# Kernel optimization log

Measured on AMD Instinct MI355X. Metric: run time of the kernel, lower is better.

Reference implementation:

```python
import jax, jax.numpy as jnp
import numpy as np
import math

D_MODEL = 32
N_HEADS = 2
FEAT_DIM = 16
HEAD_DIM = 16  # d_model // num_key_value_heads
EPS = 1e-12
R2 = math.sqrt(2.0)
RD = math.sqrt(FEAT_DIM)
RRD = math.sqrt(RD)


def taylor_exp(x):
    # x: (b, h, l, f) -> (b, h, l, 1 + f + f*f)
    b, h, l, f = x.shape
    x2 = (x[..., :, None] * x[..., None, :]).reshape(b, h, l, f * f) / R2
    term1 = jnp.ones_like(x[..., :1])
    term2 = x / RRD
    term3 = x2 / RD
    return jnp.concatenate([term1, term2, term3], axis=-1)


def setup_inputs() -> dict:
    key = jax.random.key(0)
    ks = jax.random.split(key, 5)
    b, l = 4, 2048
    return {
        "hidden_states": jax.random.normal(ks[0], (b, l, D_MODEL), dtype=jnp.float32),
        "Wq": jax.random.normal(ks[1], (FEAT_DIM * N_HEADS, D_MODEL), dtype=jnp.float32) * (1.0 / math.sqrt(D_MODEL)),
        "Wk": jax.random.normal(ks[2], (FEAT_DIM * N_HEADS, D_MODEL), dtype=jnp.float32) * (1.0 / math.sqrt(D_MODEL)),
        "Wv": jax.random.normal(ks[3], (N_HEADS * HEAD_DIM, D_MODEL), dtype=jnp.float32) * (1.0 / math.sqrt(D_MODEL)),
        "Wo": jax.random.normal(ks[4], (D_MODEL, N_HEADS * HEAD_DIM), dtype=jnp.float32) * (1.0 / math.sqrt(D_MODEL)),
    }


def reference(hidden_states, Wq, Wk, Wv, Wo):
    b, l, _ = hidden_states.shape
    # projections (nn.Linear: x @ W.T)
    q = (hidden_states @ Wq.T).reshape(b, l, N_HEADS, FEAT_DIM).transpose(0, 2, 1, 3)  # (b,h,l,f)
    k = (hidden_states @ Wk.T).reshape(b, l, N_HEADS, FEAT_DIM).transpose(0, 2, 1, 3)
    v = (hidden_states @ Wv.T).reshape(b, l, N_HEADS, HEAD_DIM).transpose(0, 2, 1, 3)  # (b,h,l,d)

    q = taylor_exp(q)  # (b,h,l,D) with D = 1+f+f^2 = 273
    k = taylor_exp(k)

    # causal linear attention: num_t = q_t . sum_{s<=t} k_s v_s^T
    kv = jnp.cumsum(k[..., None, :] * v[..., :, None], axis=2)  # (b,h,l,d,D)
    num = jnp.einsum('bhlD,bhldD->bhld', q, kv)                  # (b,h,l,d)
    denom = jnp.einsum('bhlD,bhlD->bhl', q, jnp.cumsum(k, axis=2)) + EPS
    y = num / denom[..., None]

    y = y.transpose(0, 2, 1, 3).reshape(b, l, N_HEADS * HEAD_DIM)  # (b,l,h*d)
    return (y @ Wo.T).astype(hidden_states.dtype)
```

## Files before the change

kernel.cpp:

```cpp
#include <hip/hip_runtime.h>
#include <math.h>

#define B 4
#define H 2
#define L 2048
#define DM 32
#define F 16
#define HD 16
#define DD 273
#define CHK 64
#define NC (L / CHK)
#define BH (B * H)

#define SC_LIN 0.5f
#define SC_QUAD 0.17677669529663687f

__global__ __launch_bounds__(256) void chunksum_kernel(
    const float* __restrict__ hs, const float* __restrict__ Wq,
    const float* __restrict__ Wk, const float* __restrict__ Wv,
    float* __restrict__ qp, float* __restrict__ kp, float* __restrict__ vp,
    float* __restrict__ S_kv, float* __restrict__ S_k) {
  int blk = blockIdx.x;
  int bh = blk >> 5, ch = blk & (NC - 1);
  int b = bh >> 1, h = bh & 1;
  int lane = threadIdx.x & 63, wave = threadIdx.x >> 6;
  int l = ch * CHK + lane;

  __shared__ float ks[CHK][F + 1];
  __shared__ float vs[CHK][F];

  float x[DM];
  const float4* xr = (const float4*)(hs + ((size_t)b * L + l) * DM);
#pragma unroll
  for (int j = 0; j < DM / 4; j++) {
    float4 v = xr[j];
    x[4 * j] = v.x; x[4 * j + 1] = v.y; x[4 * j + 2] = v.z; x[4 * j + 3] = v.w;
  }
  for (int c = wave * 12; c < wave * 12 + 12; c++) {
    int kind = c >> 4;
    int f = c & 15;
    const float* __restrict__ W = (kind == 0) ? Wq : (kind == 1) ? Wk : Wv;
    const float* wr = W + (size_t)(h * 16 + f) * DM;
    float acc = 0.f;
#pragma unroll
    for (int i = 0; i < DM; i++) acc += x[i] * wr[i];
    float* dst = (kind == 0) ? qp : (kind == 1) ? kp : vp;
    dst[((size_t)bh * L + l) * F + f] = acc;
    if (kind == 1) ks[lane][f] = acc;
    if (kind == 2) vs[lane][f] = acc;
  }
  if (threadIdx.x < CHK) ks[threadIdx.x][16] = 1.0f;
  __syncthreads();

#pragma unroll
  for (int rep = 0; rep < 2; rep++) {
    int dd = threadIdx.x + rep * 256;
    if (dd >= DD) break;
    int i, j;
    float sc;
    if (dd == 0) {
      i = 16; j = 16; sc = 1.0f;
    } else if (dd <= F) {
      i = dd - 1; j = 16; sc = SC_LIN;
    } else {
      int m = dd - 17;
      i = m >> 4; j = m & 15; sc = SC_QUAD;
    }
    float acc[HD];
#pragma unroll
    for (int hh = 0; hh < HD; hh++) acc[hh] = 0.f;
    float acck = 0.f;
    for (int p = 0; p < CHK; p++) {
      float kf = sc * ks[p][i] * ks[p][j];
      acck += kf;
      const float4* vr = (const float4*)vs[p];
#pragma unroll
      for (int h4 = 0; h4 < 4; h4++) {
        float4 v = vr[h4];
        acc[4 * h4] += kf * v.x;
        acc[4 * h4 + 1] += kf * v.y;
        acc[4 * h4 + 2] += kf * v.z;
        acc[4 * h4 + 3] += kf * v.w;
      }
    }
    float* dst = S_kv + ((size_t)blk * DD + dd) * HD;
#pragma unroll
    for (int hh = 0; hh < HD; hh++) dst[hh] = acc[hh];
    S_k[(size_t)blk * DD + dd] = acck;
  }
}

#define PSLICES 19
__global__ __launch_bounds__(256) void prefix_kernel(float* __restrict__ S_kv,
                                                     float* __restrict__ S_k) {
  int blk = blockIdx.x;
  int bh = blk / PSLICES, sl = blk % PSLICES;
  int e = sl * 256 + threadIdx.x;
  if (e < DD * HD) {
    size_t base = (size_t)bh * NC * DD * HD + e;
    float v[NC];
#pragma unroll
    for (int c = 0; c < NC; c++) v[c] = S_kv[base + (size_t)c * DD * HD];
    float run = 0.f;
#pragma unroll
    for (int c = 0; c < NC; c++) {
      S_kv[base + (size_t)c * DD * HD] = run;
      run += v[c];
    }
  } else if (e < DD * HD + DD) {
    int e2 = e - DD * HD;
    size_t base = (size_t)bh * NC * DD + e2;
    float v[NC];
#pragma unroll
    for (int c = 0; c < NC; c++) v[c] = S_k[base + (size_t)c * DD];
    float run = 0.f;
#pragma unroll
    for (int c = 0; c < NC; c++) {
      S_k[base + (size_t)c * DD] = run;
      run += v[c];
    }
  }
}

__global__ __launch_bounds__(256) void outchunk_kernel(
    const float* __restrict__ qp, const float* __restrict__ kp,
    const float* __restrict__ vp, const float* __restrict__ St_kv,
    const float* __restrict__ St_k, float* __restrict__ y) {
  int blk = blockIdx.x;
  int bh = blk >> 5, ch = blk & (NC - 1);
  int b = bh >> 1, h = bh & 1;
  int t = threadIdx.x & 63;
  int u = threadIdx.x >> 6;

  __shared__ float qs[CHK][F + 1];
  __shared__ float ks[CHK][F];
  __shared__ float vs[CHK][F];
  __shared__ float S[DD][HD];
  __shared__ float Sk[DD + 3];
  __shared__ float red[4][CHK][20];

  const float4* qb = (const float4*)(qp + ((size_t)bh * L + (size_t)ch * CHK) * F);
  const float4* kb = (const float4*)(kp + ((size_t)bh * L + (size_t)ch * CHK) * F);
  const float4* vb = (const float4*)(vp + ((size_t)bh * L + (size_t)ch * CHK) * F);
  {
    int r = threadIdx.x >> 2, c4 = (threadIdx.x & 3) * 4;
    float4 v = qb[threadIdx.x];
    qs[r][c4] = v.x; qs[r][c4 + 1] = v.y; qs[r][c4 + 2] = v.z; qs[r][c4 + 3] = v.w;
    ((float4*)ks)[threadIdx.x] = kb[threadIdx.x];
    ((float4*)vs)[threadIdx.x] = vb[threadIdx.x];
  }
  if (threadIdx.x < CHK) qs[threadIdx.x][16] = 1.0f;
  const float4* Sb = (const float4*)(St_kv + (size_t)blk * DD * HD);
  for (int i = threadIdx.x; i < DD * HD / 4; i += 256) ((float4*)S)[i] = Sb[i];
  const float* Skb = St_k + (size_t)blk * DD;
  for (int i = threadIdx.x; i < DD; i += 256) Sk[i] = Skb[i];

  float qreg[F];
  const float4* qrow = (const float4*)(qp + ((size_t)bh * L + (size_t)ch * CHK + t) * F);
#pragma unroll
  for (int j = 0; j < 4; j++) {
    float4 v = qrow[j];
    qreg[4 * j] = v.x; qreg[4 * j + 1] = v.y;
    qreg[4 * j + 2] = v.z; qreg[4 * j + 3] = v.w;
  }
  __syncthreads();

  float acc[HD];
#pragma unroll
  for (int hh = 0; hh < HD; hh++) acc[hh] = 0.f;
  float den = 0.f;

  for (int dd = u; dd < DD; dd += 4) {
    float phi;
    if (dd == 0) {
      phi = 1.0f;
    } else if (dd <= F) {
      phi = qs[t][dd - 1] * SC_LIN;
    } else {
      int m = dd - 17;
      phi = qs[t][m >> 4] * qs[t][m & 15] * SC_QUAD;
    }
    den += phi * Sk[dd];
    const float4* Sr = (const float4*)S[dd];
#pragma unroll
    for (int j4 = 0; j4 < 4; j4++) {
      float4 sv = Sr[j4];
      acc[4 * j4] += phi * sv.x;
      acc[4 * j4 + 1] += phi * sv.y;
      acc[4 * j4 + 2] += phi * sv.z;
      acc[4 * j4 + 3] += phi * sv.w;
    }
  }

#pragma unroll
  for (int m = 0; m < CHK / 4; m++) {
    int s = u + 4 * m;
    const float4* kr = (const float4*)ks[s];
    float dot = 0.f;
#pragma unroll
    for (int i4 = 0; i4 < 4; i4++) {
      float4 kv = kr[i4];
      dot += qreg[4 * i4] * kv.x + qreg[4 * i4 + 1] * kv.y +
             qreg[4 * i4 + 2] * kv.z + qreg[4 * i4 + 3] * kv.w;
    }
    float scv = 1.0f + dot * 0.25f + dot * dot * 0.03125f;
    scv = (s <= t) ? scv : 0.0f;
    den += scv;
    const float4* vr = (const float4*)vs[s];
#pragma unroll
    for (int h4 = 0; h4 < 4; h4++) {
      float4 v = vr[h4];
      acc[4 * h4] += scv * v.x;
      acc[4 * h4 + 1] += scv * v.y;
      acc[4 * h4 + 2] += scv * v.z;
      acc[4 * h4 + 3] += scv * v.w;
    }
  }

#pragma unroll
  for (int hh = 0; hh < HD; hh++) red[u][t][hh] = acc[hh];
  red[u][t][16] = den;
  __syncthreads();

  for (int idx = threadIdx.x; idx < CHK * 17; idx += 256) {
    int t2 = idx / 17, e = idx % 17;
    red[0][t2][e] =
        red[0][t2][e] + red[1][t2][e] + red[2][t2][e] + red[3][t2][e];
  }
  __syncthreads();

  if (threadIdx.x < CHK) {
    int t2 = threadIdx.x;
    float inv = 1.0f / (red[0][t2][16] + 1e-12f);
    float* yb = y + (((size_t)(b * L + ch * CHK + t2)) * H + h) * HD;
#pragma unroll
    for (int hh = 0; hh < HD; hh++) yb[hh] = red[0][t2][hh] * inv;
  }
}

__global__ __launch_bounds__(256) void out_kernel(const float* __restrict__ y,
                                                  const float* __restrict__ Wo,
                                                  float* __restrict__ out) {
  int lane = threadIdx.x & 63;
  int wave = threadIdx.x >> 6;
  int row = blockIdx.x * 64 + lane;
  float yr[DM];
  const float4* yb = (const float4*)(y + (size_t)row * DM);
#pragma unroll
  for (int j = 0; j < DM / 4; j++) {
    float4 v = yb[j];
    yr[4 * j] = v.x; yr[4 * j + 1] = v.y; yr[4 * j + 2] = v.z; yr[4 * j + 3] = v.w;
  }
  for (int c = wave * 8; c < wave * 8 + 8; c++) {
    float acc = 0.f;
#pragma unroll
    for (int i = 0; i < DM; i++) acc += yr[i] * Wo[c * DM + i];
    out[(size_t)row * DM + c] = acc;
  }
}

extern "C" void kernel_launch(void* const* d_in, const int* in_sizes, int n_in,
                              void* d_out, int out_size, void* d_ws,
                              size_t ws_size, hipStream_t stream) {
  const float* hs = (const float*)d_in[0];
  const float* Wq = (const float*)d_in[1];
  const float* Wk = (const float*)d_in[2];
  const float* Wv = (const float*)d_in[3];
  const float* Wo = (const float*)d_in[4];
  float* out = (float*)d_out;

  float* ws = (float*)d_ws;
  float* qp = ws;
  float* kp = qp + (size_t)BH * L * F;
  float* vp = kp + (size_t)BH * L * F;
  float* S_kv = vp + (size_t)BH * L * F;
  float* S_k = S_kv + (size_t)BH * NC * DD * HD;
  float* y = S_k + (size_t)BH * NC * DD;

  chunksum_kernel<<<BH * NC, 256, 0, stream>>>(hs, Wq, Wk, Wv, qp, kp, vp,
                                               S_kv, S_k);
  prefix_kernel<<<BH * PSLICES, 256, 0, stream>>>(S_kv, S_k);
  outchunk_kernel<<<BH * NC, 256, 0, stream>>>(qp, kp, vp, S_kv, S_k, y);
  out_kernel<<<B * L / 64, 256, 0, stream>>>(y, Wo, out);
}
```

Measured before the change: 106.9 us.

## Split projection into own kernel and read S/k/v via uniform global loads

Moves the QKV projection out of chunksum into a separate proj_kernel that computes both heads per row, removing duplicate hidden-state reads. chunksum and outchunk now read v, k, S and Sk directly from global memory through wave-uniform addresses (readfirstlane) instead of staging them in LDS, so the loads can become scalar loads. outchunk grows to 512 threads with 8 waves splitting the DD and intra-chunk loops, which cuts LDS use and adds parallelism. The cost is an extra kernel launch and dependence on scalar-cache behaviour.

New measurement: 106.5 us. Within noise of the previous version (-0.4%).

```diff
diff --git a/kernel.cpp b/kernel.cpp
--- a/kernel.cpp
+++ b/kernel.cpp
@@ -15,42 +15,56 @@
 #define SC_LIN 0.5f
 #define SC_QUAD 0.17677669529663687f
 
-__global__ __launch_bounds__(256) void chunksum_kernel(
+__global__ __launch_bounds__(256) void proj_kernel(
     const float* __restrict__ hs, const float* __restrict__ Wq,
     const float* __restrict__ Wk, const float* __restrict__ Wv,
-    float* __restrict__ qp, float* __restrict__ kp, float* __restrict__ vp,
+    float* __restrict__ qp, float* __restrict__ kp, float* __restrict__ vp) {
+  int lane = threadIdx.x & 63;
+  int wave = __builtin_amdgcn_readfirstlane(threadIdx.x >> 6);
+  int rg = blockIdx.x >> 1;
+  int half = blockIdx.x & 1;
+  int row = rg * 64 + lane;
+  int b = row >> 11, l = row & (L - 1);
+
+  float x[DM];
+  const float4* xr = (const float4*)(hs + (size_t)row * DM);
+#pragma unroll
+  for (int j = 0; j < DM / 4; j++) {
+    float4 v = xr[j];
+    x[4 * j] = v.x; x[4 * j + 1] = v.y; x[4 * j + 2] = v.z; x[4 * j + 3] = v.w;
+  }
+  int c0 = half * 48 + wave * 12;
+  for (int c = c0; c < c0 + 12; c++) {
+    int kind = c >> 5;
+    int cc = c & 31;
+    const float* __restrict__ W = (kind == 0) ? Wq : (kind == 1) ? Wk : Wv;
+    const float* __restrict__ wr = W + (size_t)cc * DM;
+    float acc = 0.f;
+#pragma unroll
+    for (int i = 0; i < DM; i++) acc += x[i] * wr[i];
+    int h = cc >> 4, f = cc & 15;
+    float* dst = (kind == 0) ? qp : (kind == 1) ? kp : vp;
+    dst[(((size_t)(b * H + h) * L) + l) * F + f] = acc;
+  }
+}
+
+__global__ __launch_bounds__(256) void chunksum_kernel(
+    const float* __restrict__ kp, const float* __restrict__ vp,
     float* __restrict__ S_kv, float* __restrict__ S_k) {
   int blk = blockIdx.x;
   int bh = blk >> 5, ch = blk & (NC - 1);
-  int b = bh >> 1, h = bh & 1;
-  int lane = threadIdx.x & 63, wave = threadIdx.x >> 6;
-  int l = ch * CHK + lane;
-
   __shared__ float ks[CHK][F + 1];
-  __shared__ float vs[CHK][F];
-
-  float x[DM];
-  const float4* xr = (const float4*)(hs + ((size_t)b * L + l) * DM);
-#pragma unroll
-  for (int j = 0; j < DM / 4; j++) {
-    float4 v = xr[j];
-    x[4 * j] = v.x; x[4 * j + 1] = v.y; x[4 * j + 2] = v.z; x[4 * j + 3] = v.w;
-  }
-  for (int c = wave * 12; c < wave * 12 + 12; c++) {
-    int kind = c >> 4;
-    int f = c & 15;
-    const float* __restrict__ W = (kind == 0) ? Wq : (kind == 1) ? Wk : Wv;
-    const float* wr = W + (size_t)(h * 16 + f) * DM;
-    float acc = 0.f;
-#pragma unroll
-    for (int i = 0; i < DM; i++) acc += x[i] * wr[i];
-    float* dst = (kind == 0) ? qp : (kind == 1) ? kp : vp;
-    dst[((size_t)bh * L + l) * F + f] = acc;
-    if (kind == 1) ks[lane][f] = acc;
-    if (kind == 2) vs[lane][f] = acc;
+
+  const float4* kb = (const float4*)(kp + ((size_t)bh * L + (size_t)ch * CHK) * F);
+  {
+    int r = threadIdx.x >> 2, c4 = (threadIdx.x & 3) * 4;
+    float4 v = kb[threadIdx.x];
+    ks[r][c4] = v.x; ks[r][c4 + 1] = v.y; ks[r][c4 + 2] = v.z; ks[r][c4 + 3] = v.w;
   }
   if (threadIdx.x < CHK) ks[threadIdx.x][16] = 1.0f;
   __syncthreads();
+
+  const float* __restrict__ vbase = vp + ((size_t)bh * L + (size_t)ch * CHK) * F;
 
 #pragma unroll
   for (int rep = 0; rep < 2; rep++) {
@@ -73,15 +87,9 @@
     for (int p = 0; p < CHK; p++) {
       float kf = sc * ks[p][i] * ks[p][j];
       acck += kf;
-      const float4* vr = (const float4*)vs[p];
-#pragma unroll
-      for (int h4 = 0; h4 < 4; h4++) {
-        float4 v = vr[h4];
-        acc[4 * h4] += kf * v.x;
-        acc[4 * h4 + 1] += kf * v.y;
-        acc[4 * h4 + 2] += kf * v.z;
-        acc[4 * h4 + 3] += kf * v.w;
-      }
+      const float* __restrict__ vr = vbase + p * F;
+#pragma unroll
+      for (int hh = 0; hh < HD; hh++) acc[hh] += kf * vr[hh];
     }
     float* dst = S_kv + ((size_t)blk * DD + dd) * HD;
 #pragma unroll
@@ -122,7 +130,7 @@
   }
 }
 
-__global__ __launch_bounds__(256) void outchunk_kernel(
+__global__ __launch_bounds__(512) void outchunk_kernel(
     const float* __restrict__ qp, const float* __restrict__ kp,
     const float* __restrict__ vp, const float* __restrict__ St_kv,
     const float* __restrict__ St_k, float* __restrict__ y) {
@@ -130,33 +138,23 @@
   int bh = blk >> 5, ch = blk & (NC - 1);
   int b = bh >> 1, h = bh & 1;
   int t = threadIdx.x & 63;
-  int u = threadIdx.x >> 6;
+  int u = __builtin_amdgcn_readfirstlane(threadIdx.x >> 6);
 
   __shared__ float qs[CHK][F + 1];
-  __shared__ float ks[CHK][F];
-  __shared__ float vs[CHK][F];
-  __shared__ float S[DD][HD];
-  __shared__ float Sk[DD + 3];
-  __shared__ float red[4][CHK][20];
-
-  const float4* qb = (const float4*)(qp + ((size_t)bh * L + (size_t)ch * CHK) * F);
-  const float4* kb = (const float4*)(kp + ((size_t)bh * L + (size_t)ch * CHK) * F);
-  const float4* vb = (const float4*)(vp + ((size_t)bh * L + (size_t)ch * CHK) * F);
-  {
+  __shared__ float red[8][CHK][21];
+
+  if (threadIdx.x < 256) {
+    const float4* qb =
+        (const float4*)(qp + ((size_t)bh * L + (size_t)ch * CHK) * F);
     int r = threadIdx.x >> 2, c4 = (threadIdx.x & 3) * 4;
     float4 v = qb[threadIdx.x];
     qs[r][c4] = v.x; qs[r][c4 + 1] = v.y; qs[r][c4 + 2] = v.z; qs[r][c4 + 3] = v.w;
-    ((float4*)ks)[threadIdx.x] = kb[threadIdx.x];
-    ((float4*)vs)[threadIdx.x] = vb[threadIdx.x];
-  }
-  if (threadIdx.x < CHK) qs[threadIdx.x][16] = 1.0f;
-  const float4* Sb = (const float4*)(St_kv + (size_t)blk * DD * HD);
-  for (int i = threadIdx.x; i < DD * HD / 4; i += 256) ((float4*)S)[i] = Sb[i];
-  const float* Skb = St_k + (size_t)blk * DD;
-  for (int i = threadIdx.x; i < DD; i += 256) Sk[i] = Skb[i];
+    if (threadIdx.x < CHK) qs[threadIdx.x][16] = 1.0f;
+  }
 
   float qreg[F];
-  const float4* qrow = (const float4*)(qp + ((size_t)bh * L + (size_t)ch * CHK + t) * F);
+  const float4* qrow =
+      (const float4*)(qp + ((size_t)bh * L + (size_t)ch * CHK + t) * F);
 #pragma unroll
   for (int j = 0; j < 4; j++) {
     float4 v = qrow[j];
@@ -170,51 +168,42 @@
   for (int hh = 0; hh < HD; hh++) acc[hh] = 0.f;
   float den = 0.f;
 
-  for (int dd = u; dd < DD; dd += 4) {
+  const float* __restrict__ Sbase = St_kv + (size_t)blk * DD * HD;
+  const float* __restrict__ Skb = St_k + (size_t)blk * DD;
+
+  for (int m = 0; m < 35; m++) {
+    int dd = u + (m << 3);
+    if (dd >= DD) break;
     float phi;
     if (dd == 0) {
       phi = 1.0f;
     } else if (dd <= F) {
       phi = qs[t][dd - 1] * SC_LIN;
     } else {
-      int m = dd - 17;
-      phi = qs[t][m >> 4] * qs[t][m & 15] * SC_QUAD;
-    }
-    den += phi * Sk[dd];
-    const float4* Sr = (const float4*)S[dd];
-#pragma unroll
-    for (int j4 = 0; j4 < 4; j4++) {
-      float4 sv = Sr[j4];
-      acc[4 * j4] += phi * sv.x;
-      acc[4 * j4 + 1] += phi * sv.y;
-      acc[4 * j4 + 2] += phi * sv.z;
-      acc[4 * j4 + 3] += phi * sv.w;
-    }
-  }
-
-#pragma unroll
-  for (int m = 0; m < CHK / 4; m++) {
-    int s = u + 4 * m;
-    const float4* kr = (const float4*)ks[s];
+      int mm = dd - 17;
+      phi = qs[t][mm >> 4] * qs[t][mm & 15] * SC_QUAD;
+    }
+    den += phi * Skb[dd];
+    const float* __restrict__ Sr = Sbase + dd * HD;
+#pragma unroll
+    for (int jj = 0; jj < HD; jj++) acc[jj] += phi * Sr[jj];
+  }
+
+  const float* __restrict__ kbase = kp + ((size_t)bh * L + (size_t)ch * CHK) * F;
+  const float* __restrict__ vbase = vp + ((size_t)bh * L + (size_t)ch * CHK) * F;
+#pragma unroll
+  for (int mm = 0; mm < CHK / 8; mm++) {
+    int s = u + mm * 8;
+    const float* __restrict__ kr = kbase + s * F;
     float dot = 0.f;
 #pragma unroll
-    for (int i4 = 0; i4 < 4; i4++) {
-      float4 kv = kr[i4];
-      dot += qreg[4 * i4] * kv.x + qreg[4 * i4 + 1] * kv.y +
-             qreg[4 * i4 + 2] * kv.z + qreg[4 * i4 + 3] * kv.w;
-    }
+    for (int i = 0; i < F; i++) dot += qreg[i] * kr[i];
     float scv = 1.0f + dot * 0.25f + dot * dot * 0.03125f;
     scv = (s <= t) ? scv : 0.0f;
     den += scv;
-    const float4* vr = (const float4*)vs[s];
-#pragma unroll
-    for (int h4 = 0; h4 < 4; h4++) {
-      float4 v = vr[h4];
-      acc[4 * h4] += scv * v.x;
-      acc[4 * h4 + 1] += scv * v.y;
-      acc[4 * h4 + 2] += scv * v.z;
-      acc[4 * h4 + 3] += scv * v.w;
-    }
+    const float* __restrict__ vr = vbase + s * F;
+#pragma unroll
+    for (int hh = 0; hh < HD; hh++) acc[hh] += scv * vr[hh];
   }
 
 #pragma unroll
@@ -222,10 +211,12 @@
   red[u][t][16] = den;
   __syncthreads();
 
-  for (int idx = threadIdx.x; idx < CHK * 17; idx += 256) {
+  for (int idx = threadIdx.x; idx < CHK * 17; idx += 512) {
     int t2 = idx / 17, e = idx % 17;
-    red[0][t2][e] =
-        red[0][t2][e] + red[1][t2][e] + red[2][t2][e] + red[3][t2][e];
+    float sum = 0.f;
+#pragma unroll
+    for (int w = 0; w < 8; w++) sum += red[w][t2][e];
+    red[0][t2][e] = sum;
   }
   __syncthreads();
 
@@ -242,7 +233,7 @@
                                                   const float* __restrict__ Wo,
                                                   float* __restrict__ out) {
   int lane = threadIdx.x & 63;
-  int wave = threadIdx.x >> 6;
+  int wave = __builtin_amdgcn_readfirstlane(threadIdx.x >> 6);
   int row = blockIdx.x * 64 + lane;
   float yr[DM];
   const float4* yb = (const float4*)(y + (size_t)row * DM);
@@ -252,9 +243,10 @@
     yr[4 * j] = v.x; yr[4 * j + 1] = v.y; yr[4 * j + 2] = v.z; yr[4 * j + 3] = v.w;
   }
   for (int c = wave * 8; c < wave * 8 + 8; c++) {
+    const float* __restrict__ wr = Wo + (size_t)c * DM;
     float acc = 0.f;
 #pragma unroll
-    for (int i = 0; i < DM; i++) acc += yr[i] * Wo[c * DM + i];
+    for (int i = 0; i < DM; i++) acc += yr[i] * wr[i];
     out[(size_t)row * DM + c] = acc;
   }
 }
@@ -277,9 +269,9 @@
   float* S_k = S_kv + (size_t)BH * NC * DD * HD;
   float* y = S_k + (size_t)BH * NC * DD;
 
-  chunksum_kernel<<<BH * NC, 256, 0, stream>>>(hs, Wq, Wk, Wv, qp, kp, vp,
-                                               S_kv, S_k);
+  proj_kernel<<<256, 256, 0, stream>>>(hs, Wq, Wk, Wv, qp, kp, vp);
+  chunksum_kernel<<<BH * NC, 256, 0, stream>>>(kp, vp, S_kv, S_k);
   prefix_kernel<<<BH * PSLICES, 256, 0, stream>>>(S_kv, S_k);
-  outchunk_kernel<<<BH * NC, 256, 0, stream>>>(qp, kp, vp, S_kv, S_k, y);
+  outchunk_kernel<<<BH * NC, 512, 0, stream>>>(qp, kp, vp, S_kv, S_k, y);
   out_kernel<<<B * L / 64, 256, 0, stream>>>(y, Wo, out);
 }
```

## Fuse output projection into chunk kernel, processing both heads per block

Applied to the files above, without the earlier changes.

Merges the final Wo projection kernel into the per-chunk output kernel. Each 512-thread block now handles both heads of one (batch, chunk), so the full 32-wide y row is available in shared memory for the projection. The intermediate y buffer and one launch are removed. Shared-memory staging of S, Sk, k and v is replaced by direct global reads through the read-only path. This cuts LDS use and a staging barrier but relies on cache hits for the 273x16 state matrix. The grid shrinks from 256 to 128 blocks.

Result: slower. 119.3 us (+11.7%).

```diff
diff --git a/kernel.cpp b/kernel.cpp
--- a/kernel.cpp
+++ b/kernel.cpp
@@ -122,41 +122,38 @@
   }
 }
 
-__global__ __launch_bounds__(256) void outchunk_kernel(
+__global__ __launch_bounds__(512) void outchunk_kernel(
     const float* __restrict__ qp, const float* __restrict__ kp,
     const float* __restrict__ vp, const float* __restrict__ St_kv,
-    const float* __restrict__ St_k, float* __restrict__ y) {
+    const float* __restrict__ St_k, const float* __restrict__ Wo,
+    float* __restrict__ out) {
   int blk = blockIdx.x;
-  int bh = blk >> 5, ch = blk & (NC - 1);
-  int b = bh >> 1, h = bh & 1;
+  int b = blk >> 5, ch = blk & (NC - 1);
   int t = threadIdx.x & 63;
-  int u = threadIdx.x >> 6;
-
-  __shared__ float qs[CHK][F + 1];
-  __shared__ float ks[CHK][F];
-  __shared__ float vs[CHK][F];
-  __shared__ float S[DD][HD];
-  __shared__ float Sk[DD + 3];
-  __shared__ float red[4][CHK][20];
-
-  const float4* qb = (const float4*)(qp + ((size_t)bh * L + (size_t)ch * CHK) * F);
-  const float4* kb = (const float4*)(kp + ((size_t)bh * L + (size_t)ch * CHK) * F);
-  const float4* vb = (const float4*)(vp + ((size_t)bh * L + (size_t)ch * CHK) * F);
+  int wave = __builtin_amdgcn_readfirstlane(threadIdx.x >> 6);
+  int h = wave >> 2;
+  int u = wave & 3;
+  int bh = b * H + h;
+  int sblk = bh * NC + ch;
+
+  __shared__ float qs[2][CHK][F + 1];
+  __shared__ float red[8][CHK][21];
+  __shared__ float ys[CHK][DM + 1];
+
   {
-    int r = threadIdx.x >> 2, c4 = (threadIdx.x & 3) * 4;
-    float4 v = qb[threadIdx.x];
-    qs[r][c4] = v.x; qs[r][c4 + 1] = v.y; qs[r][c4 + 2] = v.z; qs[r][c4 + 3] = v.w;
-    ((float4*)ks)[threadIdx.x] = kb[threadIdx.x];
-    ((float4*)vs)[threadIdx.x] = vb[threadIdx.x];
-  }
-  if (threadIdx.x < CHK) qs[threadIdx.x][16] = 1.0f;
-  const float4* Sb = (const float4*)(St_kv + (size_t)blk * DD * HD);
-  for (int i = threadIdx.x; i < DD * HD / 4; i += 256) ((float4*)S)[i] = Sb[i];
-  const float* Skb = St_k + (size_t)blk * DD;
-  for (int i = threadIdx.x; i < DD; i += 256) Sk[i] = Skb[i];
+    int i = threadIdx.x;
+    int h2 = i >> 8, r = (i >> 2) & 63, c4 = (i & 3) * 4;
+    const float4* qb =
+        (const float4*)(qp + ((size_t)(b * H + h2) * L + (size_t)ch * CHK) * F);
+    float4 v = qb[i & 255];
+    qs[h2][r][c4] = v.x; qs[h2][r][c4 + 1] = v.y;
+    qs[h2][r][c4 + 2] = v.z; qs[h2][r][c4 + 3] = v.w;
+    if (i < 2 * CHK) qs[i >> 6][i & 63][16] = 1.0f;
+  }
 
   float qreg[F];
-  const float4* qrow = (const float4*)(qp + ((size_t)bh * L + (size_t)ch * CHK + t) * F);
+  const float4* qrow =
+      (const float4*)(qp + ((size_t)bh * L + (size_t)ch * CHK + t) * F);
 #pragma unroll
   for (int j = 0; j < 4; j++) {
     float4 v = qrow[j];
@@ -170,92 +167,70 @@
   for (int hh = 0; hh < HD; hh++) acc[hh] = 0.f;
   float den = 0.f;
 
-  for (int dd = u; dd < DD; dd += 4) {
+  const float* __restrict__ Sbase = St_kv + (size_t)sblk * DD * HD;
+  const float* __restrict__ Skb = St_k + (size_t)sblk * DD;
+
+  for (int m = 0; m < 69; m++) {
+    int dd = u + (m << 2);
+    if (dd >= DD) break;
     float phi;
     if (dd == 0) {
       phi = 1.0f;
     } else if (dd <= F) {
-      phi = qs[t][dd - 1] * SC_LIN;
+      phi = qs[h][t][dd - 1] * SC_LIN;
     } else {
-      int m = dd - 17;
-      phi = qs[t][m >> 4] * qs[t][m & 15] * SC_QUAD;
-    }
-    den += phi * Sk[dd];
-    const float4* Sr = (const float4*)S[dd];
-#pragma unroll
-    for (int j4 = 0; j4 < 4; j4++) {
-      float4 sv = Sr[j4];
-      acc[4 * j4] += phi * sv.x;
-      acc[4 * j4 + 1] += phi * sv.y;
-      acc[4 * j4 + 2] += phi * sv.z;
-      acc[4 * j4 + 3] += phi * sv.w;
-    }
-  }
-
-#pragma unroll
-  for (int m = 0; m < CHK / 4; m++) {
-    int s = u + 4 * m;
-    const float4* kr = (const float4*)ks[s];
+      int mm = dd - 17;
+      phi = qs[h][t][mm >> 4] * qs[h][t][mm & 15] * SC_QUAD;
+    }
+    den += phi * Skb[dd];
+    const float* __restrict__ Sr = Sbase + dd * HD;
+#pragma unroll
+    for (int jj = 0; jj < HD; jj++) acc[jj] += phi * Sr[jj];
+  }
+
+  const float* __restrict__ kbase =
+      kp + ((size_t)bh * L + (size_t)ch * CHK) * F;
+  const float* __restrict__ vbase =
+      vp + ((size_t)bh * L + (size_t)ch * CHK) * F;
+#pragma unroll
+  for (int mm = 0; mm < CHK / 4; mm++) {
+    int s = u + mm * 4;
+    const float* __restrict__ kr = kbase + s * F;
     float dot = 0.f;
 #pragma unroll
-    for (int i4 = 0; i4 < 4; i4++) {
-      float4 kv = kr[i4];
-      dot += qreg[4 * i4] * kv.x + qreg[4 * i4 + 1] * kv.y +
-             qreg[4 * i4 + 2] * kv.z + qreg[4 * i4 + 3] * kv.w;
-    }
+    for (int i = 0; i < F; i++) dot += qreg[i] * kr[i];
     float scv = 1.0f + dot * 0.25f + dot * dot * 0.03125f;
     scv = (s <= t) ? scv : 0.0f;
     den += scv;
-    const float4* vr = (const float4*)vs[s];
-#pragma unroll
-    for (int h4 = 0; h4 < 4; h4++) {
-      float4 v = vr[h4];
-      acc[4 * h4] += scv * v.x;
-      acc[4 * h4 + 1] += scv * v.y;
-      acc[4 * h4 + 2] += scv * v.z;
-      acc[4 * h4 + 3] += scv * v.w;
-    }
-  }
-
-#pragma unroll
-  for (int hh = 0; hh < HD; hh++) red[u][t][hh] = acc[hh];
-  red[u][t][16] = den;
-  __syncthreads();
-
-  for (int idx = threadIdx.x; idx < CHK * 17; idx += 256) {
-    int t2 = idx / 17, e = idx % 17;
-    red[0][t2][e] =
-        red[0][t2][e] + red[1][t2][e] + red[2][t2][e] + red[3][t2][e];
-  }
-  __syncthreads();
-
-  if (threadIdx.x < CHK) {
-    int t2 = threadIdx.x;
-    float inv = 1.0f / (red[0][t2][16] + 1e-12f);
-    float* yb = y + (((size_t)(b * L + ch * CHK + t2)) * H + h) * HD;
-#pragma unroll
-    for (int hh = 0; hh < HD; hh++) yb[hh] = red[0][t2][hh] * inv;
-  }
-}
-
-__global__ __launch_bounds__(256) void out_kernel(const float* __restrict__ y,
-                                                  const float* __restrict__ Wo,
-                                                  float* __restrict__ out) {
-  int lane = threadIdx.x & 63;
-  int wave = threadIdx.x >> 6;
-  int row = blockIdx.x * 64 + lane;
-  float yr[DM];
-  const float4* yb = (const float4*)(y + (size_t)row * DM);
-#pragma unroll
-  for (int j = 0; j < DM / 4; j++) {
-    float4 v = yb[j];
-    yr[4 * j] = v.x; yr[4 * j + 1] = v.y; yr[4 * j + 2] = v.z; yr[4 * j + 3] = v.w;
-  }
-  for (int c = wave * 8; c < wave * 8 + 8; c++) {
-    float acc = 0.f;
-#pragma unroll
-    for (int i = 0; i < DM; i++) acc += yr[i] * Wo[c * DM + i];
-    out[(size_t)row * DM + c] = acc;
+    const float* __restrict__ vr = vbase + s * F;
+#pragma unroll
+    for (int hh = 0; hh < HD; hh++) acc[hh] += scv * vr[hh];
+  }
+
+#pragma unroll
+  for (int hh = 0; hh < HD; hh++) red[wave][t][hh] = acc[hh];
+  red[wave][t][16] = den;
+  __syncthreads();
+
+  for (int idx = threadIdx.x; idx < CHK * DM; idx += 512) {
+    int t2 = idx >> 5, c = idx & 31;
+    int h2 = c >> 4, hh = c & 15, w0 = h2 * 4;
+    float num = red[w0][t2][hh] + red[w0 + 1][t2][hh] + red[w0 + 2][t2][hh] +
+                red[w0 + 3][t2][hh];
+    float dn = red[w0][t2][16] + red[w0 + 1][t2][16] + red[w0 + 2][t2][16] +
+               red[w0 + 3][t2][16];
+    ys[t2][c] = num / (dn + 1e-12f);
+  }
+  __syncthreads();
+
+#pragma unroll
+  for (int q = 0; q < 4; q++) {
+    int oc = wave * 4 + q;
+    const float* __restrict__ wr = Wo + (size_t)oc * DM;
+    float acc2 = 0.f;
+#pragma unroll
+    for (int c = 0; c < DM; c++) acc2 += ys[t][c] * wr[c];
+    out[((size_t)(b * L + ch * CHK + t)) * DM + oc] = acc2;
   }
 }
 
@@ -275,11 +250,9 @@
   float* vp = kp + (size_t)BH * L * F;
   float* S_kv = vp + (size_t)BH * L * F;
   float* S_k = S_kv + (size_t)BH * NC * DD * HD;
-  float* y = S_k + (size_t)BH * NC * DD;
 
   chunksum_kernel<<<BH * NC, 256, 0, stream>>>(hs, Wq, Wk, Wv, qp, kp, vp,
                                                S_kv, S_k);
   prefix_kernel<<<BH * PSLICES, 256, 0, stream>>>(S_kv, S_k);
-  outchunk_kernel<<<BH * NC, 256, 0, stream>>>(qp, kp, vp, S_kv, S_k, y);
-  out_kernel<<<B * L / 64, 256, 0, stream>>>(y, Wo, out);
-}
+  outchunk_kernel<<<B * NC, 512, 0, stream>>>(qp, kp, vp, S_kv, S_k, Wo, out);
+}
```
